# Kernel optimization log

Measured on AMD Instinct MI355X. Metric: run time of the kernel, lower is better.

## Reference

```python
import jax, jax.numpy as jnp
import numpy as np

BS, N, DX, DE, DY, NH = 4, 256, 256, 64, 128, 8
DF = DX // NH
ORDER = 3


def layer_norm(x, g, b, eps=1e-6):
    m = jnp.mean(x, -1, keepdims=True)
    v = jnp.mean((x - m) ** 2, -1, keepdims=True)
    return (x - m) / jnp.sqrt(v + eps) * g + b


def setup_inputs() -> dict:
    key = jax.random.key(0)
    ks = jax.random.split(key, 32)
    s = 0.02
    p = {}
    p['X'] = jax.random.normal(ks[0], (BS, N, DX), jnp.float32)
    p['E'] = jax.random.normal(ks[1], (BS, N, N, DE), jnp.float32)
    p['y'] = jax.random.normal(ks[2], (BS, DY), jnp.float32)
    lens = jax.random.randint(ks[3], (BS,), N // 2, N + 1)
    p['node_mask'] = (jnp.arange(N)[None, :] < lens[:, None]).astype(jnp.int32)
    p['W_emax'] = s * jax.random.normal(ks[4], (DE, DX))
    p['W_x1'] = s * jax.random.normal(ks[5], (DX, DX))
    p['Wq'] = s * jax.random.normal(ks[6], (DX, DX))
    p['Wk'] = s * jax.random.normal(ks[7], (DX, DX))
    p['Wv'] = s * jax.random.normal(ks[8], (DX, DX))
    p['Wo'] = s * jax.random.normal(ks[9], (DX, DX))
    p['W_y2'] = s * jax.random.normal(ks[10], (DY, DX))
    p['W_x2'] = s * jax.random.normal(ks[11], (DX, DX))
    p['Wc'] = s * jax.random.normal(ks[12], (DY, ORDER))
    p['bc'] = jnp.zeros((ORDER,), jnp.float32)
    p['sim_alpha'] = 0.1 * jax.random.normal(ks[13], (1,))
    p['W_Eout'] = s * jax.random.normal(ks[14], (DE, DE))
    p['G_kernel'] = 0.01 * jax.random.normal(ks[15], (DE, 128))
    p['X_kernel'] = 0.01 * jax.random.normal(ks[16], (DX, 64))
    p['W_Gtrans'] = s * jax.random.normal(ks[17], (128 * DE, DY))
    p['W_Xtrans'] = s * jax.random.normal(ks[18], (64 * DX, DY))
    p['W_yout'] = s * jax.random.normal(ks[19], (DY, DY))
    p['gx'] = jnp.ones((DX,), jnp.float32); p['bx'] = jnp.zeros((DX,), jnp.float32)
    p['ge'] = jnp.ones((DE,), jnp.float32); p['be'] = jnp.zeros((DE,), jnp.float32)
    p['gy'] = jnp.ones((DY,), jnp.float32); p['by'] = jnp.zeros((DY,), jnp.float32)
    return p


def reference(X, E, y, node_mask, W_emax, W_x1, Wq, Wk, Wv, Wo, W_y2, W_x2, Wc, bc,
              sim_alpha, W_Eout, G_kernel, X_kernel, W_Gtrans, W_Xtrans, W_yout,
              gx, bx, ge, be, gy, by):
    bs, n, dx = X.shape
    de = E.shape[-1]
    nm = node_mask.astype(X.dtype)              # bs, n
    x_mask = nm[:, :, None]                     # bs, n, 1
    emask = x_mask[:, :, None, :] * x_mask[:, None, :, :]  # bs, n, n, 1

    # --- edge -> node encoding (masked mean over dim 2; torch mean divides by n) ---
    e_enc = jax.nn.relu(jnp.mean(jnp.einsum('bijd,df->bijf', E, W_emax) * emask, axis=2))
    xplus = (X + jax.nn.relu(e_enc @ W_x1)) * x_mask

    # --- masked multi-head self attention (dropout = identity in eval) ---
    q = (xplus @ Wq).reshape(bs, n, NH, DF)
    k = (xplus @ Wk).reshape(bs, n, NH, DF)
    v = (xplus @ Wv).reshape(bs, n, NH, DF)
    scores = jnp.einsum('bqhd,bkhd->bhqk', q, k) / (DF ** 0.5)
    scores = jnp.where(nm[:, None, None, :] > 0, scores, -1e9)
    attn_out = jnp.einsum('bhqk,bkhd->bqhd', jax.nn.softmax(scores, -1), v).reshape(bs, n, dx) @ Wo
    new_X = layer_norm(attn_out * x_mask + X, gx, bx)

    # --- similarity-augmented edge matrix + order-3 polynomial recurrence ---
    xplusy = jax.nn.relu((X + jax.nn.relu(y @ W_y2)[:, None, :]) @ W_x2)
    sim = jnp.einsum('bnd,bmd->bnm', xplusy, xplusy) / (dx ** 0.5)
    G = (sim_alpha * sim[..., None] + E) * emask          # bs, n, n, de
    Gr = G.reshape(bs, de, n, n)                          # raw reshape, exactly as torch
    coeff = y @ Wc + bc                                    # bs, 3
    newE = coeff[:, 0][:, None, None, None] * Gr
    for kk in range(1, ORDER):
        newE = jnp.matmul(Gr, newE) + coeff[:, kk][:, None, None, None] * Gr
    new_E = layer_norm(jax.nn.relu(newE.reshape(bs, n, n, de) @ W_Eout) * emask + E, ge, be)

    # --- masked softmax pooling over edges ---
    Em = E * emask
    lg = jnp.where(emask > 0, (Em @ G_kernel) / (de ** 0.5), -1e9)   # bs,n,n,128
    aG = jax.nn.softmax(lg.reshape(bs, n * n, -1), axis=1)            # bs,n^2,128
    G_enc = jnp.einsum('bpk,bpd->bkd', aG, Em.reshape(bs, n * n, de)).reshape(bs, -1)
    G_enc = jax.nn.relu(G_enc @ W_Gtrans)

    # --- masked softmax pooling over nodes ---
    Xm = x_mask * X
    lx = jnp.where(x_mask > 0, (Xm @ X_kernel) / (dx ** 0.5), -1e9)   # bs,n,64
    aX = jax.nn.softmax(lx, axis=1)
    X_enc = jnp.einsum('bnk,bnd->bkd', aX, Xm).reshape(bs, -1)
    X_enc = jax.nn.relu(X_enc @ W_Xtrans)

    new_y = layer_norm(jax.nn.relu((G_enc + X_enc) @ W_yout) + y, gy, by)
    return new_X, new_E, new_y
```

## Files before the change

kernel.cpp:

```cpp
#include <hip/hip_runtime.h>
#include <hip/hip_bf16.h>

typedef __hip_bfloat16 bf16;
__device__ __forceinline__ bf16 tobf(float v){ return __float2bfloat16(v); }
__device__ __forceinline__ float frombf(bf16 v){ return __bfloat162float(v); }
__device__ __forceinline__ short f2bs(float x){ bf16 h=tobf(x); return *reinterpret_cast<short*>(&h); }
__device__ __forceinline__ float bs2f(short s){ unsigned int v=((unsigned int)(unsigned short)s)<<16; return __int_as_float((int)v); }

typedef __attribute__((ext_vector_type(8))) short bf16x8;
typedef __attribute__((ext_vector_type(4))) short short4v;
typedef __attribute__((ext_vector_type(4))) float f32x4;
typedef __attribute__((ext_vector_type(4))) int int4v;

static constexpr int cB=4, cN=256, cDX=256, cDE=64, cDY=128, cNH=8, cDF=32;

static constexpr size_t F_SIM  = 0;
static constexpr size_t F_P    = 262144;
static constexpr size_t F_NP   = 2359296;
static constexpr size_t F_GP   = F_NP + 1048576;
static constexpr size_t F_XP   = F_NP + 1048576 + 32768;
static constexpr size_t F_S    = 6619136;
static constexpr size_t F_EENC = 6684672;
static constexpr size_t F_XPL  = 6946816;
static constexpr size_t F_QB   = 7208960;
static constexpr size_t F_KB   = 7471104;
static constexpr size_t F_VB   = 7733248;
static constexpr size_t F_YW   = 7995392;
static constexpr size_t F_XPY  = 7996416;
static constexpr size_t F_COEF = 8258560;
static constexpr size_t F_GENC = 8258576;
static constexpr size_t F_XENC = 8291344;

__global__ void k_coeff_yw(const float* y, const float* Wc, const float* bc,
                           const float* W_y2, float* coeff, float* yw){
  int b = blockIdx.x; int f = threadIdx.x;
  float acc = 0.f;
  for(int r=0;r<cDY;++r) acc += y[b*cDY+r]*W_y2[r*cDX+f];
  yw[b*cDX+f] = fmaxf(acc,0.f);
  if (f < 3){
    float c = bc[f];
    for(int r=0;r<cDY;++r) c += y[b*cDY+r]*Wc[r*3+f];
    coeff[b*3+f] = c;
  }
}

__global__ void __launch_bounds__(256) k_reduceE(const float* E, const int* nm, float* S){
  int bi = blockIdx.x; int b = bi / cN;
  int t = threadIdx.x;
  int seg = t&15;
  int rg  = t>>4;
  const float* Eb = E + (size_t)bi*cN*cDE;
  f32x4 acc = (f32x4){0.f,0.f,0.f,0.f};
  for(int j=rg;j<cN;j+=16){
    float m = (float)nm[b*cN+j];
    f32x4 v = *(const f32x4*)&Eb[j*cDE + seg*4];
    acc[0]+=v[0]*m; acc[1]+=v[1]*m; acc[2]+=v[2]*m; acc[3]+=v[3]*m;
  }
  __shared__ f32x4 red[16][16];
  red[rg][seg]=acc; __syncthreads();
  for(int st=8;st>0;st>>=1){
    if(rg<st){
      f32x4 o=red[rg+st][seg];
      f32x4 s=red[rg][seg];
      s[0]+=o[0]; s[1]+=o[1]; s[2]+=o[2]; s[3]+=o[3];
      red[rg][seg]=s;
    }
    __syncthreads();
  }
  if(rg==0) *(f32x4*)&S[(size_t)bi*cDE + seg*4]=red[0][seg];
}

__global__ void k_eenc(const float* S, const float* W_emax, const int* nm, float* eenc){
  int bi = blockIdx.x; int b = bi/cN; int i = bi%cN;
  int f = threadIdx.x;
  __shared__ float s[cDE];
  if (f<cDE) s[f]=S[(size_t)bi*cDE+f];
  __syncthreads();
  float acc=0.f;
  for(int d=0;d<cDE;++d) acc += s[d]*W_emax[d*cDX+f];
  float mi=(float)nm[b*cN+i];
  eenc[(size_t)bi*cDX+f] = fmaxf(acc*mi*(1.f/cN), 0.f);
}

__global__ void k_xplus(const float* X, const float* eenc, const float* W_x1,
                        const int* nm, float* xplus){
  int bi=blockIdx.x; int b=bi/cN; int i=bi%cN;
  int f=threadIdx.x;
  __shared__ float row[cDX];
  row[f]=eenc[(size_t)bi*cDX+f];
  __syncthreads();
  float acc=0.f;
  for(int c=0;c<cDX;++c) acc += row[c]*W_x1[c*cDX+f];
  float mi=(float)nm[b*cN+i];
  xplus[(size_t)bi*cDX+f] = (X[(size_t)bi*cDX+f] + fmaxf(acc,0.f))*mi;
}

__global__ void k_qkv(const float* xplus, const float* Wq, const float* Wk, const float* Wv,
                      float* qb, float* kb, float* vb){
  int bi=blockIdx.x; int f=threadIdx.x;
  __shared__ float row[cDX];
  row[f]=xplus[(size_t)bi*cDX+f];
  __syncthreads();
  float aq=0,ak=0,av=0;
  for(int c=0;c<cDX;++c){ float r=row[c]; aq+=r*Wq[c*cDX+f]; ak+=r*Wk[c*cDX+f]; av+=r*Wv[c*cDX+f]; }
  qb[(size_t)bi*cDX+f]=aq; kb[(size_t)bi*cDX+f]=ak; vb[(size_t)bi*cDX+f]=av;
}

__global__ void k_attn_softmax(const float* qb, const float* kb, const int* nm, float* P){
  int id=blockIdx.x; int b=id/(cNH*cN); int rem=id%(cNH*cN); int h=rem/cN; int i=rem%cN;
  int j=threadIdx.x;
  __shared__ float qrow[cDF];
  if (j<cDF) qrow[j]=qb[((size_t)b*cN+i)*cDX + h*cDF + j];
  __syncthreads();
  const float* krow = kb + ((size_t)b*cN+j)*cDX + h*cDF;
  float s=0.f;
  for(int c=0;c<cDF;++c) s += qrow[c]*krow[c];
  s *= 0.17677669529663687f;
  float val = (nm[b*cN+j]>0) ? s : -1e9f;
  __shared__ float red[256];
  red[j]=val; __syncthreads();
  for(int st=128;st>0;st>>=1){ if(j<st) red[j]=fmaxf(red[j],red[j+st]); __syncthreads(); }
  float mx=red[0]; __syncthreads();
  float e=__expf(val-mx);
  red[j]=e; __syncthreads();
  for(int st=128;st>0;st>>=1){ if(j<st) red[j]+=red[j+st]; __syncthreads(); }
  float denom=red[0];
  P[(size_t)id*cN + j] = e/denom;
}

__global__ void k_attn_out(const float* P, const float* vb, const float* Wo,
                           const float* X, const int* nm, const float* gx, const float* bx,
                           float* newX){
  int bi=blockIdx.x; int b=bi/cN; int i=bi%cN;
  int t=threadIdx.x;
  __shared__ float p8[cNH][cN];
  for(int h=0;h<cNH;++h) p8[h][t]=P[(((size_t)b*cNH+h)*cN+i)*cN + t];
  __syncthreads();
  int h=t/cDF;
  float acc=0.f;
  for(int j=0;j<cN;++j) acc += p8[h][j]*vb[((size_t)b*cN+j)*cDX + t];
  __shared__ float arow[cDX];
  arow[t]=acc; __syncthreads();
  float o=0.f;
  for(int c=0;c<cDX;++c) o += arow[c]*Wo[c*cDX+t];
  float mi=(float)nm[b*cN+i];
  float v = o*mi + X[(size_t)bi*cDX+t];
  __shared__ float red[256];
  red[t]=v; __syncthreads();
  for(int st=128;st>0;st>>=1){ if(t<st) red[t]+=red[t+st]; __syncthreads(); }
  float mean=red[0]*(1.f/cDX); __syncthreads();
  float dv=v-mean;
  red[t]=dv*dv; __syncthreads();
  for(int st=128;st>0;st>>=1){ if(t<st) red[t]+=red[t+st]; __syncthreads(); }
  float var=red[0]*(1.f/cDX);
  newX[(size_t)bi*cDX+t]=dv*rsqrtf(var+1e-6f)*gx[t]+bx[t];
}

__global__ void k_xplusy(const float* X, const float* yw, const float* W_x2, float* xpy){
  int bi=blockIdx.x; int b=bi/cN;
  int f=threadIdx.x;
  __shared__ float row[cDX];
  row[f]=X[(size_t)bi*cDX+f]+yw[b*cDX+f];
  __syncthreads();
  float acc=0.f;
  for(int c=0;c<cDX;++c) acc += row[c]*W_x2[c*cDX+f];
  xpy[(size_t)bi*cDX+f]=fmaxf(acc,0.f);
}

__global__ void k_sim(const float* xp, float* sim){
  int b=blockIdx.z;
  int tx=threadIdx.x, ty=threadIdx.y;
  __shared__ float Aa[16][17], Bb[16][17];
  const float* base = xp + (size_t)b*cN*cDX;
  float acc=0.f;
  for(int kt=0;kt<cDX;kt+=16){
    Aa[ty][tx]=base[(size_t)(blockIdx.y*16+ty)*cDX + kt+tx];
    Bb[ty][tx]=base[(size_t)(blockIdx.x*16+ty)*cDX + kt+tx];
    __syncthreads();
    for(int c=0;c<16;++c) acc += Aa[ty][c]*Bb[tx][c];
    __syncthreads();
  }
  sim[((size_t)b*cN + blockIdx.y*16+ty)*cN + blockIdx.x*16+tx] = acc*(1.f/16.f);
}

__global__ void k_G(const float* E, const float* sim, const int* nm, const float* alpha_p,
                    bf16* G){
  int bi=blockIdx.x; int b=bi/cN; int i=bi%cN;
  float mi=(float)nm[b*cN+i];
  float alpha=alpha_p[0];
  size_t base=(size_t)bi*cN*cDE;
  for(int t=threadIdx.x;t<cN*cDE;t+=blockDim.x){
    int j=t>>6;
    float mj=(float)nm[b*cN+j];
    G[base+t]=tobf((alpha*sim[(size_t)bi*cN+j]+E[base+t])*mi*mj);
  }
}

__global__ void __launch_bounds__(256) k_transp(const short* G, short* Gt){
  const int bc=blockIdx.z;
  const int p0=blockIdx.y*128, q0=blockIdx.x*128;
  const int t=threadIdx.x;
  __shared__ short T[128][136];
  const short* src=G+(size_t)bc*65536;
  short* dst=Gt+(size_t)bc*65536;
#pragma unroll
  for(int l=0;l<8;++l){
    int idx=t+l*256;
    int r=idx>>4, seg=idx&15;
    *(int4v*)&T[r][seg*8]=*(const int4v*)&src[(size_t)(p0+r)*256 + q0 + seg*8];
  }
  __syncthreads();
  int qq=t&127, hf=t>>7;
#pragma unroll
  for(int ss=0;ss<8;++ss){
    bf16x8 v;
#pragma unroll
    for(int ii=0;ii<8;++ii) v[ii]=T[hf*64+ss*8+ii][qq];
    *(bf16x8*)&dst[(size_t)(q0+qq)*256 + p0 + hf*64 + ss*8]=v;
  }
}

__global__ void __launch_bounds__(256) k_bmm_t(const short* G, const short* Gt, short* Bt2,
                                               const float* coeff){
  const int bc=blockIdx.z; const int b=bc>>6;
  const float alpha=coeff[b*3+0];
  const float beta=coeff[b*3+1];
  const short* Ag=G+(size_t)bc*65536;
  const short* At=Gt+(size_t)bc*65536;
  short* Ct=Bt2+(size_t)bc*65536;
  const int row0=blockIdx.y*128, col0=blockIdx.x*128;
  const int t=threadIdx.x;
  const int lane=t&63, w=t>>6;
  const int wr=w>>1, wc=w&1;
  const int l15=lane&15, l4=lane>>4;
  __shared__ char smem[36864];
  short (*A_s)[72]=(short(*)[72])smem;
  short (*B_s)[72]=(short(*)[72])(smem+18432);
  float (*Cf)[132]=(float(*)[132])smem;
  f32x4 acc[4][4];
#pragma unroll
  for(int m=0;m<4;++m)
#pragma unroll
    for(int n=0;n<4;++n) acc[m][n]=(f32x4){0.f,0.f,0.f,0.f};

  for(int kt=0;kt<256;kt+=64){
#pragma unroll
    for(int l=0;l<4;++l){
      int idx=t+l*256;
      int r=idx>>3, seg=idx&7;
      *(int4v*)&A_s[r][seg*8]=*(const int4v*)&Ag[(size_t)(row0+r)*256 + kt + seg*8];
      *(int4v*)&B_s[r][seg*8]=*(const int4v*)&At[(size_t)(col0+r)*256 + kt + seg*8];
    }
    __syncthreads();
#pragma unroll
    for(int ks=0;ks<64;ks+=32){
      bf16x8 am[4], bn[4];
#pragma unroll
      for(int m=0;m<4;++m) am[m]=*(const bf16x8*)&A_s[wr*64+m*16+l15][ks+l4*8];
#pragma unroll
      for(int n=0;n<4;++n) bn[n]=*(const bf16x8*)&B_s[wc*64+n*16+l15][ks+l4*8];
#pragma unroll
      for(int m=0;m<4;++m)
#pragma unroll
        for(int n=0;n<4;++n)
          acc[m][n]=__builtin_amdgcn_mfma_f32_16x16x32_bf16(am[m],bn[n],acc[m][n],0,0,0);
    }
    __syncthreads();
  }
  for(int rs=0;rs<8;++rs){
    if(rs) __syncthreads();
    int m=rs&3;
    if(wr==(rs>>2)){
#pragma unroll
      for(int n=0;n<4;++n)
#pragma unroll
        for(int r=0;r<4;++r)
          Cf[l4*4+r][wc*64+n*16+l15]=acc[m][n][r];
    }
    __syncthreads();
    int c=t>>1, hf=t&1;
    const short* gsrc=&At[(size_t)(col0+c)*256 + row0 + rs*16 + hf*8];
    short* dst=&Ct[(size_t)(col0+c)*256 + row0 + rs*16 + hf*8];
    bf16x8 a8=*(const bf16x8*)gsrc;
    bf16x8 o8;
#pragma unroll
    for(int ii=0;ii<8;++ii)
      o8[ii]=f2bs(alpha*Cf[hf*8+ii][c] + beta*bs2f(a8[ii]));
    *(bf16x8*)dst=o8;
  }
}

__global__ void __launch_bounds__(256) k_bmm_f(const short* G, const short* Bt2, short* Cbf,
                                               const float* coeff){
  const int bc=blockIdx.z; const int b=bc>>6;
  const float beta=coeff[b*3+2];
  const short* Ag=G+(size_t)bc*65536;
  const short* Bt=Bt2+(size_t)bc*65536;
  short* Cb=Cbf+(size_t)bc*65536;
  const int row0=blockIdx.y*128, col0=blockIdx.x*128;
  const int t=threadIdx.x;
  const int lane=t&63, w=t>>6;
  const int wr=w>>1, wc=w&1;
  const int l15=lane&15, l4=lane>>4;
  __shared__ char smem[36864];
  short (*A_s)[72]=(short(*)[72])smem;
  short (*B_s)[72]=(short(*)[72])(smem+18432);
  float (*Cf)[132]=(float(*)[132])smem;
  f32x4 acc[4][4];
#pragma unroll
  for(int m=0;m<4;++m)
#pragma unroll
    for(int n=0;n<4;++n) acc[m][n]=(f32x4){0.f,0.f,0.f,0.f};

  for(int kt=0;kt<256;kt+=64){
#pragma unroll
    for(int l=0;l<4;++l){
      int idx=t+l*256;
      int r=idx>>3, seg=idx&7;
      *(int4v*)&A_s[r][seg*8]=*(const int4v*)&Ag[(size_t)(row0+r)*256 + kt + seg*8];
      *(int4v*)&B_s[r][seg*8]=*(const int4v*)&Bt[(size_t)(col0+r)*256 + kt + seg*8];
    }
    __syncthreads();
#pragma unroll
    for(int ks=0;ks<64;ks+=32){
      bf16x8 am[4], bn[4];
#pragma unroll
      for(int m=0;m<4;++m) am[m]=*(const bf16x8*)&A_s[wr*64+m*16+l15][ks+l4*8];
#pragma unroll
      for(int n=0;n<4;++n) bn[n]=*(const bf16x8*)&B_s[wc*64+n*16+l15][ks+l4*8];
#pragma unroll
      for(int m=0;m<4;++m)
#pragma unroll
        for(int n=0;n<4;++n)
          acc[m][n]=__builtin_amdgcn_mfma_f32_16x16x32_bf16(am[m],bn[n],acc[m][n],0,0,0);
    }
    __syncthreads();
  }
  for(int rs=0;rs<8;++rs){
    if(rs) __syncthreads();
    int m=rs&3;
    if(wr==(rs>>2)){
#pragma unroll
      for(int n=0;n<4;++n)
#pragma unroll
        for(int r=0;r<4;++r)
          Cf[l4*4+r][wc*64+n*16+l15]=acc[m][n][r];
    }
    __syncthreads();
    int r=t>>4, cs=t&15;
    int row=row0+rs*16+r;
    const short* asrc=&Ag[(size_t)row*256 + col0 + cs*8];
    short* dst=&Cb[(size_t)row*256 + col0 + cs*8];
    bf16x8 a8=*(const bf16x8*)asrc;
    bf16x8 o8;
#pragma unroll
    for(int ii=0;ii<8;++ii)
      o8[ii]=f2bs(Cf[r][cs*8+ii] + beta*bs2f(a8[ii]));
    *(bf16x8*)dst=o8;
  }
}

__global__ void __launch_bounds__(256) k_Eout_mfma(const short* newE_in, const float* E,
                       const int* nm, const float* W_Eout, const float* ge, const float* be,
                       float* outE){
  const int t=threadIdx.x;
  const int lane=t&63, w=t>>6;
  const int l15=lane&15, l4=lane>>4;
  const int blk=blockIdx.x;
  const int b=blk>>8, i=blk&255;
  const float mi=(float)nm[b*cN+i];
  bf16x8 bnf[2][4];
#pragma unroll
  for(int ks=0;ks<2;++ks)
#pragma unroll
    for(int n=0;n<4;++n){
      bf16x8 v;
#pragma unroll
      for(int ii=0;ii<8;++ii)
        v[ii]=f2bs(W_Eout[(ks*32+l4*8+ii)*cDE + n*16+l15]);
      bnf[ks][n]=v;
    }
  float gev[4], bev[4];
#pragma unroll
  for(int n=0;n<4;++n){ gev[n]=ge[n*16+l15]; bev[n]=be[n*16+l15]; }

  for(int it=0;it<4;++it){
    const int j0=it*64+w*16;
    const int p0=blk*256 + j0;
    f32x4 acc[4];
#pragma unroll
    for(int n=0;n<4;++n) acc[n]=(f32x4){0.f,0.f,0.f,0.f};
    if(mi>0.f){
#pragma unroll
      for(int ks=0;ks<2;++ks){
        bf16x8 am=*(const bf16x8*)&newE_in[(size_t)(p0+l15)*cDE + ks*32 + l4*8];
#pragma unroll
        for(int n=0;n<4;++n)
          acc[n]=__builtin_amdgcn_mfma_f32_16x16x32_bf16(am,bnf[ks][n],acc[n],0,0,0);
      }
    }
    float mj[4];
#pragma unroll
    for(int r=0;r<4;++r) mj[r]=mi*(float)nm[b*cN + j0 + l4*4 + r];
#pragma unroll
    for(int reg=0;reg<4;++reg){
      size_t rowoff=(size_t)(p0 + l4*4 + reg)*cDE;
      float v0=fmaxf(acc[0][reg],0.f)*mj[reg]+E[rowoff + 0*16+l15];
      float v1=fmaxf(acc[1][reg],0.f)*mj[reg]+E[rowoff + 1*16+l15];
      float v2=fmaxf(acc[2][reg],0.f)*mj[reg]+E[rowoff + 2*16+l15];
      float v3=fmaxf(acc[3][reg],0.f)*mj[reg]+E[rowoff + 3*16+l15];
      float s=v0+v1+v2+v3;
      float q=v0*v0+v1*v1+v2*v2+v3*v3;
#pragma unroll
      for(int m=1;m<16;m<<=1){ s+=__shfl_xor(s,m); q+=__shfl_xor(q,m); }
      float mean=s*(1.f/cDE);
      float var=q*(1.f/cDE)-mean*mean;
      float inv=rsqrtf(var+1e-6f);
      outE[rowoff + 0*16+l15]=(v0-mean)*inv*gev[0]+bev[0];
      outE[rowoff + 1*16+l15]=(v1-mean)*inv*gev[1]+bev[1];
      outE[rowoff + 2*16+l15]=(v2-mean)*inv*gev[2]+bev[2];
      outE[rowoff + 3*16+l15]=(v3-mean)*inv*gev[3]+bev[3];
    }
  }
}

__global__ void __launch_bounds__(256) k_Gaccum_mfma(const float* E, const int* nm,
                                                     const float* G_kernel,
                                                     float* Npart, float* Dpart){
  const int chunk=blockIdx.x;
  const int b=blockIdx.y;
  const int t=threadIdx.x;
  const int lane=t&63, w=t>>6;
  const int l15=lane&15, l4=lane>>4;

  __shared__ short EmA[128][72];
  __shared__ short EmT[64][136];
  __shared__ short Wt[128][136];
  __shared__ float mrow[128];
  __shared__ float Dacc[128];
  __shared__ float Dpar[4][128];

  bf16x8 gk[2][8];
#pragma unroll
  for(int kt=0;kt<2;++kt)
#pragma unroll
    for(int n=0;n<8;++n){
      bf16x8 v;
#pragma unroll
      for(int ii=0;ii<8;++ii)
        v[ii]=f2bs(G_kernel[(kt*32+l4*8+ii)*128 + n*16+l15]*0.125f);
      gk[kt][n]=v;
    }

  f32x4 nacc[2][4];
#pragma unroll
  for(int a=0;a<2;++a)
#pragma unroll
    for(int d2=0;d2<4;++d2) nacc[a][d2]=(f32x4){0.f,0.f,0.f,0.f};

  if(t<128) Dacc[t]=0.f;
  __syncthreads();

  const size_t ebase=((size_t)b)<<16;
  for(int sub=0;sub<4;++sub){
    const int rowbase = chunk*512 + sub*128;
    {
      int pr=t>>1, hh=t&1;
      int p=rowbase+pr;
      const float* src=&E[(ebase+p)*cDE + hh*32];
#pragma unroll
      for(int q=0;q<8;++q){
        float4 v=*(const float4*)(src+q*4);
        short4v s4; s4[0]=f2bs(v.x); s4[1]=f2bs(v.y); s4[2]=f2bs(v.z); s4[3]=f2bs(v.w);
        *(short4v*)&EmA[pr][hh*32+q*4]=s4;
        EmT[hh*32+q*4+0][pr]=s4[0];
        EmT[hh*32+q*4+1][pr]=s4[1];
        EmT[hh*32+q*4+2][pr]=s4[2];
        EmT[hh*32+q*4+3][pr]=s4[3];
      }
      if(hh==0) mrow[pr]=(float)(nm[b*cN+(p>>8)]*nm[b*cN+(p&255)]);
    }
    __syncthreads();

    f32x4 wacc[2][8];
#pragma unroll
    for(int m=0;m<2;++m)
#pragma unroll
      for(int n=0;n<8;++n) wacc[m][n]=(f32x4){0.f,0.f,0.f,0.f};
#pragma unroll
    for(int kt=0;kt<2;++kt){
      bf16x8 am[2];
#pragma unroll
      for(int m=0;m<2;++m) am[m]=*(const bf16x8*)&EmA[w*32+m*16+l15][kt*32+l4*8];
#pragma unroll
      for(int m=0;m<2;++m)
#pragma unroll
        for(int n=0;n<8;++n)
          wacc[m][n]=__builtin_amdgcn_mfma_f32_16x16x32_bf16(am[m],gk[kt][n],wacc[m][n],0,0,0);
    }
    float dsum[8];
#pragma unroll
    for(int n=0;n<8;++n) dsum[n]=0.f;
#pragma unroll
    for(int m=0;m<2;++m){
#pragma unroll
      for(int r=0;r<4;++r){
        int pl=w*32+m*16+l4*4+r;
        float mv=mrow[pl];
#pragma unroll
        for(int n=0;n<8;++n){
          float wv=(mv>0.f)?__expf(wacc[m][n][r]):0.f;
          dsum[n]+=wv;
          Wt[n*16+l15][pl]=f2bs(wv);
        }
      }
    }
#pragma unroll
    for(int n=0;n<8;++n){
      float s=dsum[n];
      s+=__shfl_xor(s,16); s+=__shfl_xor(s,32);
      if(l4==0) Dpar[w][n*16+l15]=s;
    }
    __syncthreads();

#pragma unroll
    for(int ks=0;ks<4;++ks){
      bf16x8 aw[2];
#pragma unroll
      for(int a=0;a<2;++a) aw[a]=*(const bf16x8*)&Wt[w*32+a*16+l15][ks*32+l4*8];
      bf16x8 bm[4];
#pragma unroll
      for(int d2=0;d2<4;++d2)
        bm[d2]=*(const bf16x8*)&EmT[d2*16+l15][ks*32+l4*8];
#pragma unroll
      for(int a=0;a<2;++a)
#pragma unroll
        for(int d2=0;d2<4;++d2)
          nacc[a][d2]=__builtin_amdgcn_mfma_f32_16x16x32_bf16(aw[a],bm[d2],nacc[a][d2],0,0,0);
    }
    __syncthreads();
    if(t<128) Dacc[t]+=Dpar[0][t]+Dpar[1][t]+Dpar[2][t]+Dpar[3][t];
    __syncthreads();
  }

  size_t pi=(size_t)b*128+chunk;
  float* np=Npart + pi*128*cDE;
#pragma unroll
  for(int a=0;a<2;++a){
#pragma unroll
    for(int d2=0;d2<4;++d2){
#pragma unroll
      for(int r=0;r<4;++r){
        int k=w*32+a*16+l4*4+r;
        int d=d2*16+l15;
        np[(size_t)k*cDE+d]=nacc[a][d2][r];
      }
    }
  }
  if(t<128) Dpart[pi*128+t]=Dacc[t];
}

__global__ void k_Gcombine(const float* Npart, const float* Dpart, float* Genc){
  int bk=blockIdx.x; int b=bk>>7; int k=bk&127;
  int d=threadIdx.x;
  float n=0.f, dd=0.f;
  for(int pi=0;pi<128;++pi){
    size_t base=((size_t)b*128+pi)*128+k;
    n += Npart[base*cDE+d];
    dd += Dpart[base];
  }
  Genc[(size_t)b*8192 + k*cDE + d]=n/dd;
}

__global__ void k_Xenc(const float* X, const int* nm, const float* X_kernel, float* Xenc){
  int k=blockIdx.x;
  int b=blockIdx.y;
  int n=threadIdx.x;
  float m=(float)nm[b*cN+n];
  const float* xr=X+((size_t)b*cN+n)*cDX;
  float acc=0.f;
  for(int c=0;c<cDX;++c) acc += xr[c]*X_kernel[c*64+k];
  float lg=(m>0.f)?acc*(1.f/16.f):-1e9f;
  __shared__ float red[256];
  red[n]=lg; __syncthreads();
  for(int st=128;st>0;st>>=1){ if(n<st) red[n]=fmaxf(red[n],red[n+st]); __syncthreads(); }
  float mx=red[0]; __syncthreads();
  float e=__expf(lg-mx);
  red[n]=e; __syncthreads();
  for(int st=128;st>0;st>>=1){ if(n<st) red[n]+=red[n+st]; __syncthreads(); }
  float denom=red[0]; __syncthreads();
  __shared__ float ps[256];
  ps[n]=e/denom;
  __syncthreads();
  int d=n;
  float s=0.f;
  for(int nn=0;nn<cN;++nn) s += ps[nn]*X[((size_t)b*cN+nn)*cDX+d];
  Xenc[(size_t)b*16384 + k*cDX + d]=s;
}

__global__ void __launch_bounds__(256) k_headA(const float* Genc, const float* Xenc,
                        const float* W_Gtrans, const float* W_Xtrans,
                        float* Gp, float* Xp){
  int blk=blockIdx.x;
  int t=threadIdx.x;
  int o=t&127, sub=t>>7;
  int b0=sub*2, b1=sub*2+1;
  __shared__ float ash[4][128];
  if(blk<64){
    int ch=blk;
    for(int l=t;l<512;l+=256){
      int b=l>>7, q=l&127;
      ash[b][q]=Genc[(size_t)b*8192 + ch*128 + q];
    }
    __syncthreads();
    const float* wbase=W_Gtrans + (size_t)ch*128*cDY + o;
    float a0=0.f, a1=0.f;
#pragma unroll 4
    for(int qq=0;qq<128;++qq){
      float w=wbase[(size_t)qq*cDY];
      a0+=ash[b0][qq]*w; a1+=ash[b1][qq]*w;
    }
    Gp[((size_t)b0*64+ch)*cDY+o]=a0;
    Gp[((size_t)b1*64+ch)*cDY+o]=a1;
  } else {
    int ch=blk-64;
    for(int l=t;l<512;l+=256){
      int b=l>>7, q=l&127;
      ash[b][q]=Xenc[(size_t)b*16384 + ch*128 + q];
    }
    __syncthreads();
    const float* wbase=W_Xtrans + (size_t)ch*128*cDY + o;
    float a0=0.f, a1=0.f;
#pragma unroll 4
    for(int qq=0;qq<128;++qq){
      float w=wbase[(size_t)qq*cDY];
      a0+=ash[b0][qq]*w; a1+=ash[b1][qq]*w;
    }
    Xp[((size_t)b0*128+ch)*cDY+o]=a0;
    Xp[((size_t)b1*128+ch)*cDY+o]=a1;
  }
}

__global__ void k_headB(const float* Gp, const float* Xp, const float* W_yout,
                        const float* y, const float* gy, const float* by, float* newy){
  int b=blockIdx.x; int o=threadIdx.x;
  float g=0.f,x=0.f;
  for(int ch=0;ch<64;++ch)  g+=Gp[((size_t)b*64+ch)*cDY+o];
  for(int ch=0;ch<128;++ch) x+=Xp[((size_t)b*128+ch)*cDY+o];
  __shared__ float srow[cDY];
  srow[o]=fmaxf(g,0.f)+fmaxf(x,0.f);
  __syncthreads();
  float h=0.f;
  for(int r=0;r<cDY;++r) h += srow[r]*W_yout[r*cDY+o];
  float v=fmaxf(h,0.f)+y[b*cDY+o];
  __shared__ float red[cDY];
  red[o]=v; __syncthreads();
  for(int st=64;st>0;st>>=1){ if(o<st) red[o]+=red[o+st]; __syncthreads(); }
  float mean=red[0]*(1.f/cDY); __syncthreads();
  float dv=v-mean;
  red[o]=dv*dv; __syncthreads();
  for(int st=64;st>0;st>>=1){ if(o<st) red[o]+=red[o+st]; __syncthreads(); }
  float var=red[0]*(1.f/cDY);
  newy[b*cDY+o]=dv*rsqrtf(var+1e-6f)*gy[o]+by[o];
}

extern "C" void kernel_launch(void* const* d_in, const int* in_sizes, int n_in,
                              void* d_out, int out_size, void* d_ws, size_t ws_size,
                              hipStream_t stream){
  const float* X     =(const float*)d_in[0];
  const float* E     =(const float*)d_in[1];
  const float* y     =(const float*)d_in[2];
  const int*   nm    =(const int*)  d_in[3];
  const float* W_emax=(const float*)d_in[4];
  const float* W_x1  =(const float*)d_in[5];
  const float* Wq    =(const float*)d_in[6];
  const float* Wk    =(const float*)d_in[7];
  const float* Wv    =(const float*)d_in[8];
  const float* Wo    =(const float*)d_in[9];
  const float* W_y2  =(const float*)d_in[10];
  const float* W_x2  =(const float*)d_in[11];
  const float* Wc    =(const float*)d_in[12];
  const float* bc    =(const float*)d_in[13];
  const float* salpha=(const float*)d_in[14];
  const float* W_Eout=(const float*)d_in[15];
  const float* G_kern=(const float*)d_in[16];
  const float* X_kern=(const float*)d_in[17];
  const float* W_Gtr =(const float*)d_in[18];
  const float* W_Xtr =(const float*)d_in[19];
  const float* W_yout=(const float*)d_in[20];
  const float* gx    =(const float*)d_in[21];
  const float* bx    =(const float*)d_in[22];
  const float* ge    =(const float*)d_in[23];
  const float* be    =(const float*)d_in[24];
  const float* gy    =(const float*)d_in[25];
  const float* by    =(const float*)d_in[26];

  char* wsb=(char*)d_ws;
  bf16* Gbf=(bf16*)wsb;
  short* Gs=(short*)wsb;
  short* Bt2=(short*)(wsb+33554432);
  short* Gts=(short*)(wsb+67108864);
  short* NEWEbf=(short*)(wsb+67108864);
  float* Npart=(float*)(wsb+33554432);
  float* f32=(float*)(wsb+100663296);
  float* sim  = f32+F_SIM;
  float* P    = f32+F_P;
  float* Dpart= f32+F_NP;
  float* Gp   = f32+F_GP;
  float* Xp   = f32+F_XP;
  float* S    = f32+F_S;
  float* eenc = f32+F_EENC;
  float* xplus= f32+F_XPL;
  float* qb   = f32+F_QB;
  float* kb   = f32+F_KB;
  float* vb   = f32+F_VB;
  float* yw   = f32+F_YW;
  float* xpy  = f32+F_XPY;
  float* coeff= f32+F_COEF;
  float* Genc = f32+F_GENC;
  float* Xenc = f32+F_XENC;

  float* out=(float*)d_out;
  float* newX=out;
  float* newE_out=out+262144;
  float* newy=out+17039360;

  k_coeff_yw<<<cB,256,0,stream>>>(y,Wc,bc,W_y2,coeff,yw);
  k_reduceE<<<cB*cN,256,0,stream>>>(E,nm,S);
  k_eenc<<<cB*cN,256,0,stream>>>(S,W_emax,nm,eenc);
  k_xplus<<<cB*cN,256,0,stream>>>(X,eenc,W_x1,nm,xplus);
  k_qkv<<<cB*cN,256,0,stream>>>(xplus,Wq,Wk,Wv,qb,kb,vb);
  k_attn_softmax<<<cB*cNH*cN,256,0,stream>>>(qb,kb,nm,P);
  k_attn_out<<<cB*cN,256,0,stream>>>(P,vb,Wo,X,nm,gx,bx,newX);
  k_xplusy<<<cB*cN,256,0,stream>>>(X,yw,W_x2,xpy);
  k_sim<<<dim3(16,16,cB),dim3(16,16),0,stream>>>(xpy,sim);
  k_G<<<cB*cN,256,0,stream>>>(E,sim,nm,salpha,Gbf);
  k_transp<<<dim3(2,2,cB*cDE),256,0,stream>>>(Gs,Gts);
  k_bmm_t<<<dim3(2,2,cB*cDE),256,0,stream>>>(Gs,Gts,Bt2,coeff);
  k_bmm_f<<<dim3(2,2,cB*cDE),256,0,stream>>>(Gs,Bt2,NEWEbf,coeff);
  k_Eout_mfma<<<1024,256,0,stream>>>(NEWEbf,E,nm,W_Eout,ge,be,newE_out);
  k_Gaccum_mfma<<<dim3(128,cB),256,0,stream>>>(E,nm,G_kern,Npart,Dpart);
  k_Gcombine<<<cB*128,64,0,stream>>>(Npart,Dpart,Genc);
  k_Xenc<<<dim3(64,cB),256,0,stream>>>(X,nm,X_kern,Xenc);
  k_headA<<<192,256,0,stream>>>(Genc,Xenc,W_Gtr,W_Xtr,Gp,Xp);
  k_headB<<<cB,128,0,stream>>>(Gp,Xp,W_yout,y,gy,by,newy);
}
```

Before: 385.2 us.

## Replace per-row scalar node GEMMs with tiled bf16 MFMA GEMM kernel

Replaces the one-block-per-row scalar matmul kernels (xplus, qkv, xplusy) with a templated 128x128-tiled GEMM that stages fp32 activations and weights into LDS as bf16 and computes with MFMA 16x16x32 instructions. The residual/mask and relu epilogues are fused through per-mode branches. This removes repeated uncoalesced re-reading of full weight matrices per row and moves the work onto matrix cores. In exchange, inputs are rounded to bf16, and each launch uses only 16 blocks, so fewer CUs are busy. QKV is now three separate launches instead of one fused kernel.

After: 402.2 us. 1.04x slower.

```diff
diff --git a/kernel.cpp b/kernel.cpp
--- a/kernel.cpp
+++ b/kernel.cpp
@@ -82,28 +82,101 @@
   eenc[(size_t)bi*cDX+f] = fmaxf(acc*mi*(1.f/cN), 0.f);
 }
 
-__global__ void k_xplus(const float* X, const float* eenc, const float* W_x1,
-                        const int* nm, float* xplus){
-  int bi=blockIdx.x; int b=bi/cN; int i=bi%cN;
-  int f=threadIdx.x;
-  __shared__ float row[cDX];
-  row[f]=eenc[(size_t)bi*cDX+f];
-  __syncthreads();
-  float acc=0.f;
-  for(int c=0;c<cDX;++c) acc += row[c]*W_x1[c*cDX+f];
-  float mi=(float)nm[b*cN+i];
-  xplus[(size_t)bi*cDX+f] = (X[(size_t)bi*cDX+f] + fmaxf(acc,0.f))*mi;
-}
-
-__global__ void k_qkv(const float* xplus, const float* Wq, const float* Wk, const float* Wv,
-                      float* qb, float* kb, float* vb){
-  int bi=blockIdx.x; int f=threadIdx.x;
-  __shared__ float row[cDX];
-  row[f]=xplus[(size_t)bi*cDX+f];
-  __syncthreads();
-  float aq=0,ak=0,av=0;
-  for(int c=0;c<cDX;++c){ float r=row[c]; aq+=r*Wq[c*cDX+f]; ak+=r*Wk[c*cDX+f]; av+=r*Wv[c*cDX+f]; }
-  qb[(size_t)bi*cDX+f]=aq; kb[(size_t)bi*cDX+f]=ak; vb[(size_t)bi*cDX+f]=av;
+template<int MODE>
+__global__ void __launch_bounds__(256) k_rowgemm(const float* Aact, const float* W,
+                      const float* Xres, const float* ywp, const int* nm, float* out){
+  const int row0=blockIdx.y*128, col0=blockIdx.x*128;
+  const int b=row0>>8;
+  const int t=threadIdx.x;
+  const int lane=t&63, w=t>>6;
+  const int wr=w>>1, wc=w&1;
+  const int l15=lane&15, l4=lane>>4;
+  __shared__ char smem[36864];
+  short (*A_s)[72]=(short(*)[72])smem;
+  short (*W_s)[72]=(short(*)[72])(smem+18432);
+  float (*Cf)[132]=(float(*)[132])smem;
+  f32x4 acc[4][4];
+#pragma unroll
+  for(int m=0;m<4;++m)
+#pragma unroll
+    for(int n=0;n<4;++n) acc[m][n]=(f32x4){0.f,0.f,0.f,0.f};
+
+  for(int kt=0;kt<256;kt+=64){
+#pragma unroll
+    for(int l=0;l<8;++l){
+      int idx=t+l*256;
+      int r=idx>>4, seg=idx&15;
+      float4 v=*(const float4*)&Aact[(size_t)(row0+r)*256 + kt + seg*4];
+      if(MODE==2){
+        const float* yv=&ywp[b*256 + kt + seg*4];
+        v.x+=yv[0]; v.y+=yv[1]; v.z+=yv[2]; v.w+=yv[3];
+      }
+      short4v s4; s4[0]=f2bs(v.x); s4[1]=f2bs(v.y); s4[2]=f2bs(v.z); s4[3]=f2bs(v.w);
+      *(short4v*)&A_s[r][seg*4]=s4;
+    }
+#pragma unroll
+    for(int l=0;l<8;++l){
+      int slot=t+l*256;
+      int cc4=slot>>6, k=slot&63;
+      float4 v=*(const float4*)&W[(size_t)(kt+k)*256 + col0 + cc4*4];
+      W_s[cc4*4+0][k]=f2bs(v.x);
+      W_s[cc4*4+1][k]=f2bs(v.y);
+      W_s[cc4*4+2][k]=f2bs(v.z);
+      W_s[cc4*4+3][k]=f2bs(v.w);
+    }
+    __syncthreads();
+#pragma unroll
+    for(int ks=0;ks<64;ks+=32){
+      bf16x8 am[4], bn[4];
+#pragma unroll
+      for(int m=0;m<4;++m) am[m]=*(const bf16x8*)&A_s[wr*64+m*16+l15][ks+l4*8];
+#pragma unroll
+      for(int n=0;n<4;++n) bn[n]=*(const bf16x8*)&W_s[wc*64+n*16+l15][ks+l4*8];
+#pragma unroll
+      for(int m=0;m<4;++m)
+#pragma unroll
+        for(int n=0;n<4;++n)
+          acc[m][n]=__builtin_amdgcn_mfma_f32_16x16x32_bf16(am[m],bn[n],acc[m][n],0,0,0);
+    }
+    __syncthreads();
+  }
+  for(int rs=0;rs<8;++rs){
+    if(rs) __syncthreads();
+    int m=rs&3;
+    if(wr==(rs>>2)){
+#pragma unroll
+      for(int n=0;n<4;++n)
+#pragma unroll
+        for(int r=0;r<4;++r)
+          Cf[l4*4+r][wc*64+n*16+l15]=acc[m][n][r];
+    }
+    __syncthreads();
+    int r=t>>4, cs=t&15;
+    int row=row0+rs*16+r;
+    float* dst=&out[(size_t)row*256 + col0 + cs*8];
+    f32x4 o0,o1;
+#pragma unroll
+    for(int ii=0;ii<4;++ii) o0[ii]=Cf[r][cs*8+ii];
+#pragma unroll
+    for(int ii=0;ii<4;++ii) o1[ii]=Cf[r][cs*8+4+ii];
+    if(MODE==1){
+      float mi=(float)nm[row];
+      const float* xr=&Xres[(size_t)row*256 + col0 + cs*8];
+      f32x4 x0=*(const f32x4*)xr;
+      f32x4 x1=*(const f32x4*)(xr+4);
+#pragma unroll
+      for(int ii=0;ii<4;++ii) o0[ii]=(x0[ii]+fmaxf(o0[ii],0.f))*mi;
+#pragma unroll
+      for(int ii=0;ii<4;++ii) o1[ii]=(x1[ii]+fmaxf(o1[ii],0.f))*mi;
+    } else if(MODE==2){
+#pragma unroll
+      for(int ii=0;ii<4;++ii) o0[ii]=fmaxf(o0[ii],0.f);
+#pragma unroll
+      for(int ii=0;ii<4;++ii) o1[ii]=fmaxf(o1[ii],0.f);
+    }
+    *(f32x4*)&dst[0]=o0;
+    *(f32x4*)&dst[4]=o1;
+  }
 }
 
 __global__ void k_attn_softmax(const float* qb, const float* kb, const int* nm, float* P){
@@ -154,17 +227,6 @@
   for(int st=128;st>0;st>>=1){ if(t<st) red[t]+=red[t+st]; __syncthreads(); }
   float var=red[0]*(1.f/cDX);
   newX[(size_t)bi*cDX+t]=dv*rsqrtf(var+1e-6f)*gx[t]+bx[t];
-}
-
-__global__ void k_xplusy(const float* X, const float* yw, const float* W_x2, float* xpy){
-  int bi=blockIdx.x; int b=bi/cN;
-  int f=threadIdx.x;
-  __shared__ float row[cDX];
-  row[f]=X[(size_t)bi*cDX+f]+yw[b*cDX+f];
-  __syncthreads();
-  float acc=0.f;
-  for(int c=0;c<cDX;++c) acc += row[c]*W_x2[c*cDX+f];
-  xpy[(size_t)bi*cDX+f]=fmaxf(acc,0.f);
 }
 
 __global__ void k_sim(const float* xp, float* sim){
@@ -728,11 +790,13 @@
   k_coeff_yw<<<cB,256,0,stream>>>(y,Wc,bc,W_y2,coeff,yw);
   k_reduceE<<<cB*cN,256,0,stream>>>(E,nm,S);
   k_eenc<<<cB*cN,256,0,stream>>>(S,W_emax,nm,eenc);
-  k_xplus<<<cB*cN,256,0,stream>>>(X,eenc,W_x1,nm,xplus);
-  k_qkv<<<cB*cN,256,0,stream>>>(xplus,Wq,Wk,Wv,qb,kb,vb);
+  k_rowgemm<1><<<dim3(2,8),256,0,stream>>>(eenc,W_x1,X,nullptr,nm,xplus);
+  k_rowgemm<0><<<dim3(2,8),256,0,stream>>>(xplus,Wq,nullptr,nullptr,nullptr,qb);
+  k_rowgemm<0><<<dim3(2,8),256,0,stream>>>(xplus,Wk,nullptr,nullptr,nullptr,kb);
+  k_rowgemm<0><<<dim3(2,8),256,0,stream>>>(xplus,Wv,nullptr,nullptr,nullptr,vb);
   k_attn_softmax<<<cB*cNH*cN,256,0,stream>>>(qb,kb,nm,P);
   k_attn_out<<<cB*cN,256,0,stream>>>(P,vb,Wo,X,nm,gx,bx,newX);
-  k_xplusy<<<cB*cN,256,0,stream>>>(X,yw,W_x2,xpy);
+  k_rowgemm<2><<<dim3(2,8),256,0,stream>>>(X,W_x2,nullptr,yw,nullptr,xpy);
   k_sim<<<dim3(16,16,cB),dim3(16,16),0,stream>>>(xpy,sim);
   k_G<<<cB*cN,256,0,stream>>>(E,sim,nm,salpha,Gbf);
   k_transp<<<dim3(2,2,cB*cDE),256,0,stream>>>(Gs,Gts);
```
